# Performance work log

Hardware: AMD Instinct MI355X
Metric: run time of the kernel (lower is better)

## Reference

```python
import jax, jax.numpy as jnp
import numpy as np

N = 50000      # nodes
E = 800000     # edges (before self-loops)
H = 4          # heads
C = 64         # hidden channels per head
CLS = 10       # len(bins)+1
D_IN = 64      # input feature dim
NEG_SLOPE = 0.2


def setup_inputs() -> dict:
    key = jax.random.key(0)
    ks = jax.random.split(key, 24)
    inp = {
        "x": jax.random.normal(ks[0], (N, D_IN), jnp.float32),
        "edge_index": jax.random.randint(ks[1], (2, E), 0, N),
    }
    dims = [(D_IN, C), (H * C, C), (H * C, C), (H * C, C), (H * C, CLS)]
    k = 2
    for l, (din, dout) in enumerate(dims):
        sc = 1.0 / np.sqrt(din)
        inp[f"W{l}"] = jax.random.normal(ks[k], (din, H * dout), jnp.float32) * sc; k += 1
        inp[f"as{l}"] = jax.random.normal(ks[k], (H, dout), jnp.float32) * sc; k += 1
        inp[f"ad{l}"] = jax.random.normal(ks[k], (H, dout), jnp.float32) * sc; k += 1
        inp[f"b{l}"] = jnp.zeros((H * dout,), jnp.float32)
    return inp


def gat_layer(x, src, dst, W, a_s, a_d, b):
    # PyG GATConv (concat=True): h = x W -> [N,H,Ch]
    Hh, Ch = a_s.shape
    h = (x @ W).reshape(-1, Hh, Ch)
    asn = (h * a_s).sum(-1)                      # [N,H]
    adn = (h * a_d).sum(-1)                      # [N,H]
    e = jax.nn.leaky_relu(asn[src] + adn[dst], NEG_SLOPE)   # [Et,H]
    m = jax.ops.segment_max(e, dst, num_segments=N)         # softmax over in-edges per dst
    ex = jnp.exp(e - m[dst])
    s = jax.ops.segment_sum(ex, dst, num_segments=N)
    alpha = ex / (s[dst] + 1e-16)                # [Et,H]
    out = jax.ops.segment_sum(alpha[:, :, None] * h[src], dst, num_segments=N)
    return out.reshape(-1, Hh * Ch) + b


def reference(x, edge_index, W0, as0, ad0, b0, W1, as1, ad1, b1,
              W2, as2, ad2, b2, W3, as3, ad3, b3, W4, as4, ad4, b4):
    loop = jnp.arange(N, dtype=edge_index.dtype)  # GATConv add_self_loops=True
    src = jnp.concatenate([edge_index[0], loop])
    dst = jnp.concatenate([edge_index[1], loop])
    params = [(W0, as0, ad0, b0), (W1, as1, ad1, b1), (W2, as2, ad2, b2),
              (W3, as3, ad3, b3), (W4, as4, ad4, b4)]
    for W, a_s, a_d, b in params:
        x = jax.nn.relu(gat_layer(x, src, dst, W, a_s, a_d, b))
        # dropout(p=0.5) is identity in eval mode (training=False)
    return x
```

## Files before the change

kernel.cpp:

```cpp
#include <hip/hip_runtime.h>
#include <hip/hip_bf16.h>
#include <math.h>

#define N_NODES 50000
#define N_PAD   50048
#define N_EDGES 800000
#define HEADS 4

typedef __attribute__((ext_vector_type(8))) _Float16 half8_t;
typedef __attribute__((ext_vector_type(4))) _Float16 half4_t;
typedef __attribute__((ext_vector_type(4))) float f32x4;

__device__ inline void split2(float v, _Float16& p0, _Float16& p1) {
    p0 = (_Float16)v;
    p1 = (_Float16)(v - (float)p0);
}



__global__ void init_deg_kernel(int* __restrict__ deg) {
    int i = blockIdx.x * blockDim.x + threadIdx.x;
    if (i < N_NODES) deg[i] = 1;
}

__global__ void hist_kernel(const int* __restrict__ dst, int* __restrict__ deg) {
    int i = blockIdx.x * blockDim.x + threadIdx.x;
    if (i < N_EDGES) atomicAdd(&deg[dst[i]], 1);
}

__global__ __launch_bounds__(1024) void scan_kernel(const int* __restrict__ deg,
                                                    int* __restrict__ rowptr,
                                                    int* __restrict__ cursor) {
    __shared__ int wsums[16];
    const int t = threadIdx.x;
    const int wv = t >> 6, ln = t & 63;
    const int WCHUNK = (N_NODES + 15) / 16;
    const int base = wv * WCHUNK;
    int lim = base + WCHUNK; if (lim > N_NODES) lim = N_NODES;

    int tot = 0;
    for (int i = base + ln; i < lim; i += 64) tot += deg[i];
#pragma unroll
    for (int o = 1; o < 64; o <<= 1) tot += __shfl_xor(tot, o);
    if (ln == 0) wsums[wv] = tot;
    __syncthreads();

    int run = 0;
    for (int w = 0; w < wv; ++w) run += wsums[w];

    for (int i0 = base; i0 < lim; i0 += 64) {
        int i = i0 + ln;
        int d = (i < lim) ? deg[i] : 0;
        int sc = d;
#pragma unroll
        for (int o = 1; o < 64; o <<= 1) {
            int v = __shfl_up(sc, o);
            if (ln >= o) sc += v;
        }
        if (i < lim) {
            int val = run + sc - d;
            rowptr[i] = val;
            cursor[i] = val;
        }
        run += __shfl(sc, 63);
    }
    if (t == 1023) rowptr[N_NODES] = run;
}

__global__ void scatter_kernel(const int* __restrict__ src, const int* __restrict__ dst,
                               int* __restrict__ cursor, int* __restrict__ col) {
    int i = blockIdx.x * blockDim.x + threadIdx.x;
    if (i < N_EDGES) {
        int d = dst[i];
        int pos = atomicAdd(&cursor[d], 1);
        col[pos] = src[i];
    } else if (i < N_EDGES + N_NODES) {
        int n = i - N_EDGES;
        int pos = atomicAdd(&cursor[n], 1);
        col[pos] = n;
    }
}


__global__ void x_split_kernel(const float* __restrict__ x, _Float16* __restrict__ pl,
                               size_t pstride) {
    int i = blockIdx.x * blockDim.x + threadIdx.x;
    if (i >= N_NODES * 64) return;
    int n = i >> 6, k = i & 63;
    _Float16 a, b;
    split2(x[i], a, b);
    size_t off = (size_t)(k >> 5) * ((size_t)N_PAD * 32) + (size_t)n * 32 +
                 ((((k >> 3) & 3) ^ (n & 3)) << 3) + (k & 7);
    pl[off] = a;
    pl[pstride + off] = b;
}

__global__ void w_split_kernel(const float* __restrict__ W, _Float16* __restrict__ wt,
                               int K, int NC) {
    int t = blockIdx.x * blockDim.x + threadIdx.x;
    int c = t >> 8, k = t & 255;
    float v = (k < K && c < NC) ? W[k * NC + c] : 0.f;
    _Float16 a, b;
    split2(v, a, b);
    size_t off = (size_t)(k >> 5) * 8192 + (size_t)c * 32 +
                 ((((k >> 3) & 3) ^ (c & 3)) << 3) + (k & 7);
    wt[off] = a;
    wt[65536 + off] = b;
}


template <int FUSE_ATTN>
__global__ __launch_bounds__(256) void gemm_mfma_kernel(
        const _Float16* __restrict__ Apl, size_t apstride,
        const _Float16* __restrict__ Wt,
        float* __restrict__ C, int K, int NC,
        const float* __restrict__ as_flat, const float* __restrict__ ad_flat,
        float* __restrict__ asn, float* __restrict__ adn) {
    __shared__ __align__(16) _Float16 lds[2][16384];

    const int tid = threadIdx.x;
    const int lane = tid & 63;
    const int wave = tid >> 6;
    const int wr = (wave >> 1) * 64;
    const int wc = (wave & 1) * 64;
    const int m0 = blockIdx.x * 128;
    const int n0 = blockIdx.y * 128;

    f32x4 acc[4][4];
#pragma unroll
    for (int i = 0; i < 4; ++i)
#pragma unroll
        for (int j = 0; j < 4; ++j) acc[i][j] = (f32x4){0.f, 0.f, 0.f, 0.f};

    const _Float16* gptr[8];
    size_t ktstep;
    {
        const _Float16* sbase;
        int rowbase;
        if (wave < 2) {
            sbase = Apl + (size_t)wave * apstride;
            rowbase = m0;
            ktstep = (size_t)N_PAD * 32;
        } else {
            sbase = Wt + (size_t)(wave - 2) * 65536;
            rowbase = n0;
            ktstep = 8192;
        }
#pragma unroll
        for (int it = 0; it < 8; ++it) {
            int idx = it * 64 + lane;
            gptr[it] = sbase + (size_t)(rowbase + (idx >> 2)) * 32 + (idx & 3) * 8;
        }
    }

    const int cswz = ((lane >> 4) ^ (lane & 3)) << 3;
    const int KT = K >> 5;

#pragma unroll
    for (int it = 0; it < 8; ++it) {
        __builtin_amdgcn_global_load_lds(
            (const __attribute__((address_space(1))) void*)gptr[it],
            (__attribute__((address_space(3))) void*)((char*)&lds[0][0] + wave * 8192 + it * 1024),
            16, 0, 0);
    }

    for (int kt = 0; kt < KT; ++kt) {
        __syncthreads();

        if (kt + 1 < KT) {
            char* dstw = (char*)&lds[(kt + 1) & 1][0] + wave * 8192;
#pragma unroll
            for (int it = 0; it < 8; ++it) {
                __builtin_amdgcn_global_load_lds(
                    (const __attribute__((address_space(1))) void*)(gptr[it] + (size_t)(kt + 1) * ktstep),
                    (__attribute__((address_space(3))) void*)(dstw + it * 1024),
                    16, 0, 0);
            }
        }

        const _Float16* Ab = &lds[kt & 1][0];
        const _Float16* Bb = Ab + 8192;

        half8_t bf[2][4];
#pragma unroll
        for (int p = 0; p < 2; ++p)
#pragma unroll
            for (int j = 0; j < 4; ++j) {
                int r = wc + j * 16 + (lane & 15);
                bf[p][j] = *(const half8_t*)(Bb + p * 4096 + r * 32 + cswz);
            }
#pragma unroll
        for (int i = 0; i < 4; ++i) {
            int r = wr + i * 16 + (lane & 15);
            half8_t af0 = *(const half8_t*)(Ab + r * 32 + cswz);
            half8_t af1 = *(const half8_t*)(Ab + 4096 + r * 32 + cswz);
#pragma unroll
            for (int j = 0; j < 4; ++j) {
                f32x4 c = acc[i][j];
                c = __builtin_amdgcn_mfma_f32_16x16x32_f16(af0, bf[1][j], c, 0, 0, 0);
                c = __builtin_amdgcn_mfma_f32_16x16x32_f16(af1, bf[0][j], c, 0, 0, 0);
                c = __builtin_amdgcn_mfma_f32_16x16x32_f16(af0, bf[0][j], c, 0, 0, 0);
                acc[i][j] = c;
            }
        }
    }

    const int rbase = m0 + wr + (lane >> 4) * 4;
    const int cbase = n0 + wc + (lane & 15);

    if (FUSE_ATTN) {
#pragma unroll
        for (int i = 0; i < 4; ++i)
#pragma unroll
            for (int j = 0; j < 4; ++j) {
                int gcol = cbase + j * 16;
#pragma unroll
                for (int r4 = 0; r4 < 4; ++r4) {
                    int grow = rbase + i * 16 + r4;
                    if (grow < N_NODES) C[(size_t)grow * 256 + gcol] = acc[i][j][r4];
                }
            }
        const int hd_out = (n0 + wc) >> 6;
        float as_v[4], ad_v[4];
#pragma unroll
        for (int j = 0; j < 4; ++j) {
            int gc = cbase + j * 16;
            as_v[j] = as_flat[gc];
            ad_v[j] = ad_flat[gc];
        }
#pragma unroll
        for (int i = 0; i < 4; ++i)
#pragma unroll
            for (int r4 = 0; r4 < 4; ++r4) {
                float ps = 0.f, pd = 0.f;
#pragma unroll
                for (int j = 0; j < 4; ++j) {
                    float v = acc[i][j][r4];
                    ps += v * as_v[j];
                    pd += v * ad_v[j];
                }
#pragma unroll
                for (int o = 1; o < 16; o <<= 1) {
                    ps += __shfl_xor(ps, o);
                    pd += __shfl_xor(pd, o);
                }
                if ((lane & 15) == 0) {
                    int grow = rbase + i * 16 + r4;
                    if (grow < N_NODES) {
                        asn[grow * 4 + hd_out] = ps;
                        adn[grow * 4 + hd_out] = pd;
                    }
                }
            }
    } else {
#pragma unroll
        for (int i = 0; i < 4; ++i)
#pragma unroll
            for (int j = 0; j < 4; ++j) {
                int gcol = cbase + j * 16;
                if (gcol >= NC) continue;
#pragma unroll
                for (int r4 = 0; r4 < 4; ++r4) {
                    int grow = rbase + i * 16 + r4;
                    if (grow < N_NODES) C[(size_t)grow * NC + gcol] = acc[i][j][r4];
                }
            }
    }
}


__global__ void attn_coef_kernel(const float* __restrict__ h,
                                 const float* __restrict__ a_s,
                                 const float* __restrict__ a_d,
                                 float* __restrict__ asn, float* __restrict__ adn,
                                 int CH) {
    int t = blockIdx.x * blockDim.x + threadIdx.x;
    if (t >= N_NODES * HEADS) return;
    int n = t >> 2;
    int hd = t & 3;
    const float* hp = h + (size_t)n * HEADS * CH + hd * CH;
    const float* sp = a_s + hd * CH;
    const float* dp = a_d + hd * CH;
    float s1 = 0.f, s2 = 0.f;
    for (int c = 0; c < CH; c += 2) {
        float2 hv = *reinterpret_cast<const float2*>(&hp[c]);
        float2 av = *reinterpret_cast<const float2*>(&sp[c]);
        float2 dv = *reinterpret_cast<const float2*>(&dp[c]);
        s1 += hv.x * av.x + hv.y * av.y;
        s2 += hv.x * dv.x + hv.y * dv.y;
    }
    asn[t] = s1;
    adn[t] = s2;
}


__global__ __launch_bounds__(256) void aggregate64_kernel(
        const float* __restrict__ h,
        const float* __restrict__ asn, const float* __restrict__ adn,
        const int* __restrict__ rowptr, const int* __restrict__ col,
        const float* __restrict__ bias,
        _Float16* __restrict__ pl, size_t pstride) {
    const int n = (blockIdx.x << 2) + (threadIdx.x >> 6);
    const int lane = threadIdx.x & 63;
    const int hd = lane >> 4;
    const int e16 = lane & 15;
    const int pbase = lane & 48;

    const int start = rowptr[n];
    const int end = rowptr[n + 1];
    const float adv = adn[(n << 2) | hd];

    float m = -INFINITY, s = 0.f;
    float a0 = 0.f, a1 = 0.f, a2 = 0.f, a3 = 0.f;

    for (int e0 = start; e0 < end; e0 += 16) {
        int e = e0 + e16;
        int srcl = n;
        float ev = -INFINITY;
        if (e < end) {
            srcl = col[e];
            float t = asn[(srcl << 2) | hd] + adv;
            ev = (t > 0.f) ? t : 0.2f * t;
        }
        float bm = ev;
#pragma unroll
        for (int o = 1; o < 16; o <<= 1) bm = fmaxf(bm, __shfl_xor(bm, o));
        float mn = fmaxf(m, bm);
        float scale = __expf(m - mn);
        float p = __expf(ev - mn);
        float ps = p;
#pragma unroll
        for (int o = 1; o < 16; o <<= 1) ps += __shfl_xor(ps, o);
        s = s * scale + ps;
        a0 *= scale; a1 *= scale; a2 *= scale; a3 *= scale;
        m = mn;

        int cnt = end - e0; if (cnt > 16) cnt = 16;
        int cnt4 = (cnt + 3) & ~3;
        for (int j0 = 0; j0 < cnt4; j0 += 4) {
            int sj[4]; float pj[4];
#pragma unroll
            for (int j = 0; j < 4; ++j) {
                sj[j] = __shfl(srcl, j0 + j);
                pj[j] = __shfl(p, pbase + j0 + j);
            }
            float4 hv[4];
#pragma unroll
            for (int j = 0; j < 4; ++j)
                hv[j] = *reinterpret_cast<const float4*>(h + (size_t)sj[j] * 256 + (lane << 2));
#pragma unroll
            for (int j = 0; j < 4; ++j) {
                a0 += pj[j] * hv[j].x;
                a1 += pj[j] * hv[j].y;
                a2 += pj[j] * hv[j].z;
                a3 += pj[j] * hv[j].w;
            }
        }
    }

    float sd = s + 1e-16f;
    const float* bp = bias + (lane << 2);
    float v0 = fmaxf(a0 / sd + bp[0], 0.f);
    float v1 = fmaxf(a1 / sd + bp[1], 0.f);
    float v2 = fmaxf(a2 / sd + bp[2], 0.f);
    float v3 = fmaxf(a3 / sd + bp[3], 0.f);

    _Float16 s0a, s0b, s1a, s1b, s2a, s2b, s3a, s3b;
    split2(v0, s0a, s0b);
    split2(v1, s1a, s1b);
    split2(v2, s2a, s2b);
    split2(v3, s3a, s3b);
    half4_t o0, o1;
    o0[0] = s0a; o0[1] = s1a; o0[2] = s2a; o0[3] = s3a;
    o1[0] = s0b; o1[1] = s1b; o1[2] = s2b; o1[3] = s3b;

    const int kt = lane >> 3;
    const int cp = ((lane >> 1) & 3) ^ (n & 3);
    const int inner = (lane & 1) << 2;
    size_t off = (size_t)kt * ((size_t)N_PAD * 32) + (size_t)n * 32 + (cp << 3) + inner;
    *(half4_t*)(pl + off) = o0;
    *(half4_t*)(pl + pstride + off) = o1;
}


__global__ __launch_bounds__(256) void aggregate_out10_kernel(
        const float* __restrict__ h,
        const float* __restrict__ asn, const float* __restrict__ adn,
        const int* __restrict__ rowptr, const int* __restrict__ col,
        const float* __restrict__ bias, float* __restrict__ out) {
    const int n = (blockIdx.x << 2) + (threadIdx.x >> 6);
    const int lane = threadIdx.x & 63;
    const int hd16 = lane >> 4;
    const int e16 = lane & 15;
    const bool cvalid = lane < 40;
    const int hc = ((cvalid ? lane : 0) * 205) >> 11;

    const int start = rowptr[n];
    const int end = rowptr[n + 1];
    const float adv = adn[(n << 2) | hd16];

    float m = -INFINITY, s = 0.f, a0 = 0.f, a1 = 0.f;

    for (int e0 = start; e0 < end; e0 += 16) {
        int e = e0 + e16;
        int srcl = n;
        float ev = -INFINITY;
        if (e < end) {
            srcl = col[e];
            float t = asn[(srcl << 2) | hd16] + adv;
            ev = (t > 0.f) ? t : 0.2f * t;
        }
        float bm = ev;
#pragma unroll
        for (int o = 1; o < 16; o <<= 1) bm = fmaxf(bm, __shfl_xor(bm, o));
        float mn = fmaxf(m, bm);
        float scale = __expf(m - mn);
        float p = __expf(ev - mn);
        float ps = p;
#pragma unroll
        for (int o = 1; o < 16; o <<= 1) ps += __shfl_xor(ps, o);
        s = s * scale + ps;
        m = mn;

        float sc_c = __shfl(scale, hc * 16);
        a0 *= sc_c;
        a1 *= sc_c;

        int cnt = end - e0; if (cnt > 16) cnt = 16;
        int cnt4 = (cnt + 3) & ~3;
        for (int j0 = 0; j0 < cnt4; j0 += 4) {
            int sj[4]; float pj[4];
#pragma unroll
            for (int j = 0; j < 4; ++j) {
                sj[j] = __shfl(srcl, j0 + j);
                pj[j] = __shfl(p, hc * 16 + j0 + j);
            }
            float hv[4];
#pragma unroll
            for (int j = 0; j < 4; ++j)
                hv[j] = cvalid ? h[(size_t)sj[j] * 40 + lane] : 0.f;
            a0 += pj[0] * hv[0];
            a1 += pj[1] * hv[1];
            a0 += pj[2] * hv[2];
            a1 += pj[3] * hv[3];
        }
    }

    float sd = __shfl(s, hc * 16) + 1e-16f;
    if (cvalid) {
        float v = (a0 + a1) / sd + bias[lane];
        out[(size_t)n * 40 + lane] = fmaxf(v, 0.f);
    }
}


extern "C" void kernel_launch(void* const* d_in, const int* in_sizes, int n_in,
                              void* d_out, int out_size, void* d_ws, size_t ws_size,
                              hipStream_t stream) {
    const float* x_in = (const float*)d_in[0];
    const int* ei = (const int*)d_in[1];
    const int* src = ei;
    const int* dst = ei + N_EDGES;

    const float *W[5], *AS[5], *AD[5], *BI[5];
    for (int l = 0; l < 5; ++l) {
        W[l]  = (const float*)d_in[2 + l * 4 + 0];
        AS[l] = (const float*)d_in[2 + l * 4 + 1];
        AD[l] = (const float*)d_in[2 + l * 4 + 2];
        BI[l] = (const float*)d_in[2 + l * 4 + 3];
    }

    const size_t PSTRIDE = (size_t)N_PAD * 256;
    _Float16* planes = (_Float16*)d_ws;
    float* hbuf = (float*)(planes + 2 * PSTRIDE);
    float* asn  = hbuf + (size_t)N_NODES * 256;
    float* adn  = asn + (size_t)N_NODES * HEADS;
    int* rowptr = (int*)(adn + (size_t)N_NODES * HEADS);
    int* cursor = rowptr + (N_NODES + 1);
    int* col    = cursor + N_NODES;
    _Float16* wt = (_Float16*)(((uintptr_t)(col + N_EDGES + N_NODES) + 15) & ~(uintptr_t)15);

    init_deg_kernel<<<(N_NODES + 255) / 256, 256, 0, stream>>>(cursor);
    hist_kernel<<<(N_EDGES + 255) / 256, 256, 0, stream>>>(dst, cursor);
    scan_kernel<<<1, 1024, 0, stream>>>(cursor, rowptr, cursor);
    scatter_kernel<<<(N_EDGES + N_NODES + 255) / 256, 256, 0, stream>>>(src, dst, cursor, col);

    for (int l = 0; l < 5; ++l) {
        int Kl = (l == 0) ? 64 : 256;
        int NCl = (l == 4) ? 40 : 256;
        w_split_kernel<<<256, 256, 0, stream>>>(W[l], wt + (size_t)l * 131072, Kl, NCl);
    }
    x_split_kernel<<<(N_NODES * 64 + 255) / 256, 256, 0, stream>>>(x_in, planes, PSTRIDE);

    for (int l = 0; l < 5; ++l) {
        const int K = (l == 0) ? 64 : 256;
        const int NC = (l == 4) ? 40 : 256;
        dim3 ggrid(N_PAD / 128, (NC + 127) / 128);
        const _Float16* wl = wt + (size_t)l * 131072;
        if (l < 4) {
            gemm_mfma_kernel<1><<<ggrid, 256, 0, stream>>>(
                planes, PSTRIDE, wl, hbuf, K, NC, AS[l], AD[l], asn, adn);
            aggregate64_kernel<<<N_NODES / 4, 256, 0, stream>>>(
                hbuf, asn, adn, rowptr, col, BI[l], planes, PSTRIDE);
        } else {
            gemm_mfma_kernel<0><<<ggrid, 256, 0, stream>>>(
                planes, PSTRIDE, wl, hbuf, K, NC, AS[l], AD[l], asn, adn);
            attn_coef_kernel<<<(N_NODES * HEADS + 255) / 256, 256, 0, stream>>>(
                hbuf, AS[l], AD[l], asn, adn, 10);
            aggregate_out10_kernel<<<N_NODES / 4, 256, 0, stream>>>(
                hbuf, asn, adn, rowptr, col, BI[l], (float*)d_out);
        }
    }
    (void)in_sizes; (void)n_in; (void)out_size; (void)ws_size;
}
```

Measured before the change: 842.6 us.

## Load GEMM weights from global memory directly, halve LDS, batch weight split

The GEMM kernel now stages only the A operand (node features) through LDS. All four waves share the A loads, and each wave reads its B weight fragments straight from global or L2 memory. LDS use is halved, which may allow more resident blocks, and waves whose columns fall beyond NC skip the MFMA work in the final layer. The five weight-split launches are merged into one. The trade-off is that the weight reads now depend on cache hits and their latency is no longer hidden by the LDS double buffer.

```diff
diff --git a/kernel.cpp b/kernel.cpp
--- a/kernel.cpp
+++ b/kernel.cpp
@@ -95,14 +95,20 @@
     pl[pstride + off] = b;
 }
 
-__global__ void w_split_kernel(const float* __restrict__ W, _Float16* __restrict__ wt,
-                               int K, int NC) {
+struct W5 { const float* p[5]; };
+
+__global__ void w_split_kernel(W5 ws, _Float16* __restrict__ wt) {
     int t = blockIdx.x * blockDim.x + threadIdx.x;
-    int c = t >> 8, k = t & 255;
-    float v = (k < K && c < NC) ? W[k * NC + c] : 0.f;
+    int l = t >> 16;
+    int r = t & 65535;
+    int c = r >> 8, k = r & 255;
+    int K = (l == 0) ? 64 : 256;
+    int NC = (l == 4) ? 40 : 256;
+    float v = (k < K && c < NC) ? ws.p[l][k * NC + c] : 0.f;
     _Float16 a, b;
     split2(v, a, b);
-    size_t off = (size_t)(k >> 5) * 8192 + (size_t)c * 32 +
+    size_t off = (size_t)l * 131072 +
+                 (size_t)(k >> 5) * 8192 + (size_t)c * 32 +
                  ((((k >> 3) & 3) ^ (c & 3)) << 3) + (k & 7);
     wt[off] = a;
     wt[65536 + off] = b;
@@ -116,7 +122,7 @@
         float* __restrict__ C, int K, int NC,
         const float* __restrict__ as_flat, const float* __restrict__ ad_flat,
         float* __restrict__ asn, float* __restrict__ adn) {
-    __shared__ __align__(16) _Float16 lds[2][16384];
+    __shared__ __align__(16) _Float16 lds[2][8192];
 
     const int tid = threadIdx.x;
     const int lane = tid & 63;
@@ -125,6 +131,7 @@
     const int wc = (wave & 1) * 64;
     const int m0 = blockIdx.x * 128;
     const int n0 = blockIdx.y * 128;
+    const bool wave_active = FUSE_ATTN ? true : ((n0 + wc) < NC);
 
     f32x4 acc[4][4];
 #pragma unroll
@@ -132,35 +139,26 @@
 #pragma unroll
         for (int j = 0; j < 4; ++j) acc[i][j] = (f32x4){0.f, 0.f, 0.f, 0.f};
 
-    const _Float16* gptr[8];
-    size_t ktstep;
-    {
-        const _Float16* sbase;
-        int rowbase;
-        if (wave < 2) {
-            sbase = Apl + (size_t)wave * apstride;
-            rowbase = m0;
-            ktstep = (size_t)N_PAD * 32;
-        } else {
-            sbase = Wt + (size_t)(wave - 2) * 65536;
-            rowbase = n0;
-            ktstep = 8192;
-        }
-#pragma unroll
-        for (int it = 0; it < 8; ++it) {
-            int idx = it * 64 + lane;
-            gptr[it] = sbase + (size_t)(rowbase + (idx >> 2)) * 32 + (idx & 3) * 8;
-        }
+    const size_t ktstep = (size_t)N_PAD * 32;
+    const _Float16* agsrc[4];
+    unsigned ldoff[4];
+#pragma unroll
+    for (int it = 0; it < 4; ++it) {
+        int c = wave * 4 + it;
+        int p = c >> 3, idx = c & 7;
+        agsrc[it] = Apl + (size_t)p * apstride + (size_t)m0 * 32 + idx * 512 + lane * 8;
+        ldoff[it] = (unsigned)(p * 8192 + idx * 1024);
     }
 
     const int cswz = ((lane >> 4) ^ (lane & 3)) << 3;
+    const _Float16* bfb = Wt + (size_t)(n0 + wc + (lane & 15)) * 32 + cswz;
     const int KT = K >> 5;
 
 #pragma unroll
-    for (int it = 0; it < 8; ++it) {
+    for (int it = 0; it < 4; ++it) {
         __builtin_amdgcn_global_load_lds(
-            (const __attribute__((address_space(1))) void*)gptr[it],
-            (__attribute__((address_space(3))) void*)((char*)&lds[0][0] + wave * 8192 + it * 1024),
+            (const __attribute__((address_space(1))) void*)agsrc[it],
+            (__attribute__((address_space(3))) void*)((char*)&lds[0][0] + ldoff[it]),
             16, 0, 0);
     }
 
@@ -168,39 +166,38 @@
         __syncthreads();
 
         if (kt + 1 < KT) {
-            char* dstw = (char*)&lds[(kt + 1) & 1][0] + wave * 8192;
-#pragma unroll
-            for (int it = 0; it < 8; ++it) {
+            char* dstw = (char*)&lds[(kt + 1) & 1][0];
+#pragma unroll
+            for (int it = 0; it < 4; ++it) {
                 __builtin_amdgcn_global_load_lds(
-                    (const __attribute__((address_space(1))) void*)(gptr[it] + (size_t)(kt + 1) * ktstep),
-                    (__attribute__((address_space(3))) void*)(dstw + it * 1024),
+                    (const __attribute__((address_space(1))) void*)(agsrc[it] + (size_t)(kt + 1) * ktstep),
+                    (__attribute__((address_space(3))) void*)(dstw + ldoff[it]),
                     16, 0, 0);
             }
         }
 
-        const _Float16* Ab = &lds[kt & 1][0];
-        const _Float16* Bb = Ab + 8192;
-
-        half8_t bf[2][4];
-#pragma unroll
-        for (int p = 0; p < 2; ++p)
-#pragma unroll
-            for (int j = 0; j < 4; ++j) {
-                int r = wc + j * 16 + (lane & 15);
-                bf[p][j] = *(const half8_t*)(Bb + p * 4096 + r * 32 + cswz);
-            }
-#pragma unroll
-        for (int i = 0; i < 4; ++i) {
-            int r = wr + i * 16 + (lane & 15);
-            half8_t af0 = *(const half8_t*)(Ab + r * 32 + cswz);
-            half8_t af1 = *(const half8_t*)(Ab + 4096 + r * 32 + cswz);
-#pragma unroll
-            for (int j = 0; j < 4; ++j) {
-                f32x4 c = acc[i][j];
-                c = __builtin_amdgcn_mfma_f32_16x16x32_f16(af0, bf[1][j], c, 0, 0, 0);
-                c = __builtin_amdgcn_mfma_f32_16x16x32_f16(af1, bf[0][j], c, 0, 0, 0);
-                c = __builtin_amdgcn_mfma_f32_16x16x32_f16(af0, bf[0][j], c, 0, 0, 0);
-                acc[i][j] = c;
+        if (wave_active) {
+            half8_t bf[2][4];
+#pragma unroll
+            for (int p = 0; p < 2; ++p)
+#pragma unroll
+                for (int j = 0; j < 4; ++j)
+                    bf[p][j] = *(const half8_t*)(bfb + p * 65536 + (size_t)kt * 8192 + j * 512);
+
+            const _Float16* Ab = &lds[kt & 1][0];
+#pragma unroll
+            for (int i = 0; i < 4; ++i) {
+                int r = wr + i * 16 + (lane & 15);
+                half8_t af0 = *(const half8_t*)(Ab + r * 32 + cswz);
+                half8_t af1 = *(const half8_t*)(Ab + 4096 + r * 32 + cswz);
+#pragma unroll
+                for (int j = 0; j < 4; ++j) {
+                    f32x4 c = acc[i][j];
+                    c = __builtin_amdgcn_mfma_f32_16x16x32_f16(af0, bf[1][j], c, 0, 0, 0);
+                    c = __builtin_amdgcn_mfma_f32_16x16x32_f16(af1, bf[0][j], c, 0, 0, 0);
+                    c = __builtin_amdgcn_mfma_f32_16x16x32_f16(af0, bf[0][j], c, 0, 0, 0);
+                    acc[i][j] = c;
+                }
             }
         }
     }
@@ -462,9 +459,10 @@
     const int* src = ei;
     const int* dst = ei + N_EDGES;
 
-    const float *W[5], *AS[5], *AD[5], *BI[5];
+    const float *AS[5], *AD[5], *BI[5];
+    W5 w5;
     for (int l = 0; l < 5; ++l) {
-        W[l]  = (const float*)d_in[2 + l * 4 + 0];
+        w5.p[l] = (const float*)d_in[2 + l * 4 + 0];
         AS[l] = (const float*)d_in[2 + l * 4 + 1];
         AD[l] = (const float*)d_in[2 + l * 4 + 2];
         BI[l] = (const float*)d_in[2 + l * 4 + 3];
@@ -485,11 +483,7 @@
     scan_kernel<<<1, 1024, 0, stream>>>(cursor, rowptr, cursor);
     scatter_kernel<<<(N_EDGES + N_NODES + 255) / 256, 256, 0, stream>>>(src, dst, cursor, col);
 
-    for (int l = 0; l < 5; ++l) {
-        int Kl = (l == 0) ? 64 : 256;
-        int NCl = (l == 4) ? 40 : 256;
-        w_split_kernel<<<256, 256, 0, stream>>>(W[l], wt + (size_t)l * 131072, Kl, NCl);
-    }
+    w_split_kernel<<<5 * 65536 / 256, 256, 0, stream>>>(w5, wt);
     x_split_kernel<<<(N_NODES * 64 + 255) / 256, 256, 0, stream>>>(x_in, planes, PSTRIDE);
 
     for (int l = 0; l < 5; ++l) {
```

Measured after the change: 850.5 us. About the same (+0.9%).
